# Kernel optimization log

Hardware: AMD Instinct MI355X
Metric: run time of the kernel (lower is better)

The kernel has to match this reference:

```python
import math
import jax, jax.numpy as jnp
import numpy as np

FIRE_THRESH = 0.85
DEPLETION_RATE = 0.5
EPS = 1e-12


def setup_inputs() -> dict:
    key = jax.random.key(0)
    k1, k2, k3, k4 = jax.random.split(key, 4)
    B, T, D, N = 8, 4096, 1024, 512
    x = jax.random.normal(k1, (B, T, D), dtype=jnp.float32)
    buf = jax.random.normal(k2, (N, D), dtype=jnp.float32)
    buf = buf / jnp.maximum(jnp.linalg.norm(buf, axis=-1, keepdims=True), EPS)
    depl = jax.random.uniform(k3, (N,), dtype=jnp.float32)
    hits = jax.random.randint(k4, (N,), 0, 5, dtype=jnp.int32)
    mask = jnp.ones((N,), dtype=bool)
    return {
        "x": x,
        "log_k": jnp.asarray(math.log(1.5), dtype=jnp.float32),
        "log_lambda": jnp.asarray(math.log(0.5), dtype=jnp.float32),
        "buf": buf,
        "depl": depl,
        "hits": hits,
        "mask": mask,
        "ptr": 7,
    }


def _gelu(x):
    c = math.sqrt(2.0 / math.pi)
    return 0.5 * x * (1.0 + jnp.tanh(c * (x + 0.044715 * x * x * x)))


def reference(x, log_k, log_lambda, buf, depl, hits, mask, ptr):
    k_depl = jnp.clip(jnp.exp(log_k), 0.1, 5.0)
    lam = jnp.clip(jnp.exp(log_lambda), 0.1, 3.0)

    y = _gelu(x)  # [B,T,D]
    D = x.shape[-1]
    # detached mean activation over all tokens -> [D]
    m_curr = jax.lax.stop_gradient(y).reshape(-1, D).mean(0)

    m_n = m_curr / jnp.maximum(jnp.linalg.norm(m_curr), EPS)
    buf_n = buf / jnp.maximum(jnp.linalg.norm(buf, axis=-1, keepdims=True), EPS)
    sims = jnp.where(mask, buf_n @ m_n, -1.0)  # [N]
    nearest = jnp.argmax(sims)
    max_sim = sims[nearest]
    depl_level = depl[nearest]
    h = hits[nearest].astype(y.dtype)

    # .item()-based gate in torch => no gradient through gate
    gate = jax.lax.stop_gradient(
        jnp.exp(-k_depl * (1.0 - depl_level) - lam * h)
    )
    output = y * gate

    # state update (fire, then circular write at ptr)
    fired = max_sim > FIRE_THRESH
    new_depl = depl.at[nearest].multiply(jnp.where(fired, DEPLETION_RATE, 1.0))
    new_hits = hits.at[nearest].add(jnp.where(fired, 1, 0).astype(hits.dtype))
    new_buf = buf.at[ptr].set(m_n)
    new_depl = new_depl.at[ptr].set(1.0)
    new_hits = new_hits.at[ptr].set(0)
    new_mask = mask.at[ptr].set(True)
    return output, new_buf, new_depl, new_hits, new_mask
```

## Files before the change

kernel.cpp:

```cpp
#include <hip/hip_runtime.h>
#include <math.h>

#define BT 32768
#define DD 1024
#define NN 512
#define PP 1024

__device__ __forceinline__ float fast_gelu(float x) {
    float u = 0.7978845608028654f * (x + 0.044715f * x * x * x);
    float e = __expf(2.0f * u);
    float t = 1.0f - __fdividef(2.0f, e + 1.0f);
    return 0.5f * x * (1.0f + t);
}

__global__ __launch_bounds__(256) void k_partial(const float4* __restrict__ x4,
                                                 float4* __restrict__ part) {
    int t = threadIdx.x;
    float4 acc = make_float4(0.f, 0.f, 0.f, 0.f);
    for (int row = blockIdx.x; row < BT; row += PP) {
        float4 v = x4[row * (DD / 4) + t];
        acc.x += fast_gelu(v.x);
        acc.y += fast_gelu(v.y);
        acc.z += fast_gelu(v.z);
        acc.w += fast_gelu(v.w);
    }
    part[blockIdx.x * (DD / 4) + t] = acc;
}

__global__ __launch_bounds__(256) void k_reduce1(const float* __restrict__ part,
                                                 float* __restrict__ part2) {
    int g = blockIdx.x * 256 + threadIdx.x;
    int col = g & (DD - 1);
    int chunk = g >> 10;
    float s = 0.f;
    int r0 = chunk * (PP / 16);
    for (int r = r0; r < r0 + PP / 16; ++r) s += part[r * DD + col];
    part2[chunk * DD + col] = s;
}

__global__ __launch_bounds__(1024) void k_mean_norm(const float* __restrict__ part2,
                                                    float* __restrict__ m_mean,
                                                    float* __restrict__ m_n,
                                                    float* __restrict__ nm_out) {
    int c = threadIdx.x;
    float s = 0.f;
    for (int r = 0; r < 16; ++r) s += part2[r * DD + c];
    float m = s * (1.0f / 32768.0f);
    m_mean[c] = m;
    __shared__ float red[1024];
    red[c] = m * m;
    __syncthreads();
    for (int st = 512; st > 0; st >>= 1) {
        if (c < st) red[c] += red[c + st];
        __syncthreads();
    }
    float nm = sqrtf(red[0]);
    float denom = fmaxf(nm, 1e-12f);
    m_n[c] = m / denom;
    if (c == 0) nm_out[0] = nm;
}

__global__ __launch_bounds__(256) void k_sims(const float4* __restrict__ buf4,
                                              const float4* __restrict__ m4,
                                              float* __restrict__ dot,
                                              float* __restrict__ sq) {
    int n = blockIdx.x;
    int t = threadIdx.x;
    float4 b = buf4[n * (DD / 4) + t];
    float4 m = m4[t];
    float d = b.x * m.x + b.y * m.y + b.z * m.z + b.w * m.w;
    float q = b.x * b.x + b.y * b.y + b.z * b.z + b.w * b.w;
    __shared__ float rd[256], rq[256];
    rd[t] = d;
    rq[t] = q;
    __syncthreads();
    for (int st = 128; st > 0; st >>= 1) {
        if (t < st) { rd[t] += rd[t + st]; rq[t] += rq[t + st]; }
        __syncthreads();
    }
    if (t == 0) { dot[n] = rd[0]; sq[n] = rq[0]; }
}

__global__ __launch_bounds__(512) void k_state(const float* __restrict__ dot,
                                               const float* __restrict__ sq,
                                               const float* __restrict__ nm_p,
                                               const float* __restrict__ depl,
                                               const int* __restrict__ hits,
                                               const int* __restrict__ mask,
                                               const float* __restrict__ logk_p,
                                               const float* __restrict__ loglam_p,
                                               const int* __restrict__ ptr_p,
                                               float* __restrict__ out_depl,
                                               float* __restrict__ out_hits,
                                               float* __restrict__ out_mask,
                                               float* __restrict__ gate_p) {
    int n = threadIdx.x;
    float nm = fmaxf(nm_p[0], 1e-12f);
    float nb = fmaxf(sqrtf(sq[n]), 1e-12f);
    bool mk = mask[n] != 0;
    float sim = mk ? dot[n] / (nb * nm) : -1.0f;

    __shared__ float ssim[512];
    __shared__ int sidx[512];
    ssim[n] = sim;
    sidx[n] = n;
    __syncthreads();
    for (int st = 256; st > 0; st >>= 1) {
        if (n < st) {
            float s2 = ssim[n + st];
            int i2 = sidx[n + st];
            if (s2 > ssim[n] || (s2 == ssim[n] && i2 < sidx[n])) {
                ssim[n] = s2;
                sidx[n] = i2;
            }
        }
        __syncthreads();
    }

    __shared__ int s_near, s_fired;
    if (n == 0) {
        int nearest = sidx[0];
        float msim = ssim[0];
        float k_depl = fminf(fmaxf(expf(logk_p[0]), 0.1f), 5.0f);
        float lam = fminf(fmaxf(expf(loglam_p[0]), 0.1f), 3.0f);
        float g = expf(-k_depl * (1.0f - depl[nearest]) - lam * (float)hits[nearest]);
        s_near = nearest;
        s_fired = (msim > 0.85f) ? 1 : 0;
        gate_p[0] = g;
    }
    __syncthreads();

    int ptr = ptr_p[0];
    float nd = depl[n];
    int nh = hits[n];
    float nmsk = mk ? 1.0f : 0.0f;
    if (n == s_near && s_fired) { nd *= 0.5f; nh += 1; }
    if (n == ptr) { nd = 1.0f; nh = 0; nmsk = 1.0f; }
    out_depl[n] = nd;
    out_hits[n] = (float)nh;
    out_mask[n] = nmsk;
}

__global__ __launch_bounds__(256) void k_out(const float4* __restrict__ x4,
                                             float4* __restrict__ o4,
                                             const float* __restrict__ gate_p,
                                             int n4) {
    float g = gate_p[0];
    int stride = gridDim.x * blockDim.x;
    for (int i = blockIdx.x * blockDim.x + threadIdx.x; i < n4; i += stride) {
        float4 v = x4[i];
        float4 r;
        r.x = fast_gelu(v.x) * g;
        r.y = fast_gelu(v.y) * g;
        r.z = fast_gelu(v.z) * g;
        r.w = fast_gelu(v.w) * g;
        o4[i] = r;
    }
}

__global__ __launch_bounds__(256) void k_buf(const float4* __restrict__ buf4,
                                             const float4* __restrict__ mn4,
                                             const int* __restrict__ ptr_p,
                                             float4* __restrict__ out4) {
    int i = blockIdx.x * 256 + threadIdx.x;
    int row = i >> 8;
    float4 v = (row == ptr_p[0]) ? mn4[i & 255] : buf4[i];
    out4[i] = v;
}

extern "C" void kernel_launch(void* const* d_in, const int* in_sizes, int n_in,
                              void* d_out, int out_size, void* d_ws, size_t ws_size,
                              hipStream_t stream) {
    const float* x = (const float*)d_in[0];
    const float* log_k = (const float*)d_in[1];
    const float* log_lambda = (const float*)d_in[2];
    const float* buf = (const float*)d_in[3];
    const float* depl = (const float*)d_in[4];
    const int* hits = (const int*)d_in[5];
    const int* mask = (const int*)d_in[6];
    const int* ptr = (const int*)d_in[7];

    float* out = (float*)d_out;
    float* out_buf = out + 33554432;
    float* out_depl = out_buf + NN * DD;
    float* out_hits = out_depl + NN;
    float* out_mask = out_hits + NN;

    float* ws = (float*)d_ws;
    float* part2 = ws;
    float* m_mean = ws + 16384;
    float* m_n = ws + 17408;
    float* nm = ws + 18432;
    float* gate = ws + 18433;
    float* dot = ws + 18440;
    float* sq = ws + 18952;

    float* part = out;

    k_partial<<<dim3(PP), dim3(256), 0, stream>>>((const float4*)x, (float4*)part);
    k_reduce1<<<dim3(64), dim3(256), 0, stream>>>(part, part2);
    k_mean_norm<<<dim3(1), dim3(1024), 0, stream>>>(part2, m_mean, m_n, nm);
    k_sims<<<dim3(NN), dim3(256), 0, stream>>>((const float4*)buf, (const float4*)m_mean, dot, sq);
    k_state<<<dim3(1), dim3(512), 0, stream>>>(dot, sq, nm, depl, hits, mask,
                                               log_k, log_lambda, ptr,
                                               out_depl, out_hits, out_mask, gate);
    k_out<<<dim3(2048), dim3(256), 0, stream>>>((const float4*)x, (float4*)out, gate, 8388608);
    k_buf<<<dim3(512), dim3(256), 0, stream>>>((const float4*)buf, (const float4*)m_n, ptr,
                                               (float4*)out_buf);
}
```

Measured before the change: 103.7 us.

## Fuse reduction and state kernels with last-block atomics; merge output and buffer writes

Result: slower. 138.9 us (+33.9%).

```diff
diff --git a/kernel.cpp b/kernel.cpp
--- a/kernel.cpp
+++ b/kernel.cpp
@@ -5,6 +5,8 @@
 #define DD 1024
 #define NN 512
 #define PP 1024
+
+typedef float v4f __attribute__((ext_vector_type(4)));
 
 __device__ __forceinline__ float fast_gelu(float x) {
     float u = 0.7978845608028654f * (x + 0.044715f * x * x * x);
@@ -13,12 +15,20 @@
     return 0.5f * x * (1.0f + t);
 }
 
-__global__ __launch_bounds__(256) void k_partial(const float4* __restrict__ x4,
-                                                 float4* __restrict__ part) {
+__device__ __forceinline__ void nt_store4(v4f* p, v4f v) {
+    __builtin_nontemporal_store(v, p);
+}
+
+__global__ __launch_bounds__(256) void k_partial(const v4f* __restrict__ x4,
+                                                 v4f* __restrict__ part,
+                                                 int* __restrict__ cnts) {
+    if (blockIdx.x == 0 && threadIdx.x == 0) { cnts[0] = 0; cnts[1] = 0; }
     int t = threadIdx.x;
-    float4 acc = make_float4(0.f, 0.f, 0.f, 0.f);
-    for (int row = blockIdx.x; row < BT; row += PP) {
-        float4 v = x4[row * (DD / 4) + t];
+    v4f acc = {0.f, 0.f, 0.f, 0.f};
+    int base = blockIdx.x * 32 * (DD / 4) + t;
+    #pragma unroll 4
+    for (int k = 0; k < 32; ++k) {
+        v4f v = x4[base + k * (DD / 4)];
         acc.x += fast_gelu(v.x);
         acc.y += fast_gelu(v.y);
         acc.z += fast_gelu(v.z);
@@ -27,47 +37,84 @@
     part[blockIdx.x * (DD / 4) + t] = acc;
 }
 
-__global__ __launch_bounds__(256) void k_reduce1(const float* __restrict__ part,
-                                                 float* __restrict__ part2) {
-    int g = blockIdx.x * 256 + threadIdx.x;
-    int col = g & (DD - 1);
-    int chunk = g >> 10;
-    float s = 0.f;
-    int r0 = chunk * (PP / 16);
-    for (int r = r0; r < r0 + PP / 16; ++r) s += part[r * DD + col];
-    part2[chunk * DD + col] = s;
-}
-
-__global__ __launch_bounds__(1024) void k_mean_norm(const float* __restrict__ part2,
-                                                    float* __restrict__ m_mean,
-                                                    float* __restrict__ m_n,
-                                                    float* __restrict__ nm_out) {
-    int c = threadIdx.x;
-    float s = 0.f;
-    for (int r = 0; r < 16; ++r) s += part2[r * DD + c];
-    float m = s * (1.0f / 32768.0f);
-    m_mean[c] = m;
-    __shared__ float red[1024];
-    red[c] = m * m;
-    __syncthreads();
-    for (int st = 512; st > 0; st >>= 1) {
-        if (c < st) red[c] += red[c + st];
+__global__ __launch_bounds__(256) void k_reduce_mean(const float* __restrict__ part,
+                                                     float* __restrict__ part2,
+                                                     float* __restrict__ m_mean,
+                                                     float* __restrict__ m_n,
+                                                     float* __restrict__ nm_out,
+                                                     int* __restrict__ cnts) {
+    int t = threadIdx.x, j = blockIdx.x;
+    float a0 = 0, a1 = 0, a2 = 0, a3 = 0;
+    for (int r = 0; r < 16; ++r) {
+        const float* row = part + (j * 16 + r) * DD;
+        a0 += row[t];
+        a1 += row[t + 256];
+        a2 += row[t + 512];
+        a3 += row[t + 768];
+    }
+    part2[j * DD + t] = a0;
+    part2[j * DD + t + 256] = a1;
+    part2[j * DD + t + 512] = a2;
+    part2[j * DD + t + 768] = a3;
+    __threadfence();
+    __shared__ int sLast;
+    if (t == 0) {
+        int old = __hip_atomic_fetch_add(&cnts[0], 1, __ATOMIC_ACQ_REL, __HIP_MEMORY_SCOPE_AGENT);
+        sLast = (old == 63) ? 1 : 0;
+    }
+    __syncthreads();
+    if (!sLast) return;
+    __threadfence();
+    float s0 = 0, s1 = 0, s2 = 0, s3 = 0;
+    for (int jj = 0; jj < 64; ++jj) {
+        const float* row = part2 + jj * DD;
+        s0 += row[t];
+        s1 += row[t + 256];
+        s2 += row[t + 512];
+        s3 += row[t + 768];
+    }
+    const float inv = 1.0f / 32768.0f;
+    float m0 = s0 * inv, m1 = s1 * inv, m2 = s2 * inv, m3 = s3 * inv;
+    m_mean[t] = m0;
+    m_mean[t + 256] = m1;
+    m_mean[t + 512] = m2;
+    m_mean[t + 768] = m3;
+    __shared__ float red[256];
+    red[t] = m0 * m0 + m1 * m1 + m2 * m2 + m3 * m3;
+    __syncthreads();
+    for (int st = 128; st > 0; st >>= 1) {
+        if (t < st) red[t] += red[t + st];
         __syncthreads();
     }
     float nm = sqrtf(red[0]);
-    float denom = fmaxf(nm, 1e-12f);
-    m_n[c] = m / denom;
-    if (c == 0) nm_out[0] = nm;
-}
-
-__global__ __launch_bounds__(256) void k_sims(const float4* __restrict__ buf4,
-                                              const float4* __restrict__ m4,
-                                              float* __restrict__ dot,
-                                              float* __restrict__ sq) {
-    int n = blockIdx.x;
-    int t = threadIdx.x;
-    float4 b = buf4[n * (DD / 4) + t];
-    float4 m = m4[t];
+    float den = fmaxf(nm, 1e-12f);
+    m_n[t] = m0 / den;
+    m_n[t + 256] = m1 / den;
+    m_n[t + 512] = m2 / den;
+    m_n[t + 768] = m3 / den;
+    if (t == 0) nm_out[0] = nm;
+}
+
+__global__ __launch_bounds__(256) void k_sims_state(const v4f* __restrict__ buf4,
+                                                    const float* __restrict__ m_meanf,
+                                                    const float* __restrict__ nm_p,
+                                                    const float* __restrict__ depl,
+                                                    const int* __restrict__ hits,
+                                                    const int* __restrict__ mask,
+                                                    const float* __restrict__ logk,
+                                                    const float* __restrict__ loglam,
+                                                    const int* __restrict__ ptrp,
+                                                    float* __restrict__ dot,
+                                                    float* __restrict__ sq,
+                                                    float* __restrict__ out_depl,
+                                                    float* __restrict__ out_hits,
+                                                    float* __restrict__ out_mask,
+                                                    float* __restrict__ gate_p,
+                                                    int* __restrict__ cnts) {
+    int t = threadIdx.x, n = blockIdx.x;
+    const v4f* m4 = (const v4f*)m_meanf;
+    v4f b = buf4[n * (DD / 4) + t];
+    v4f m = m4[t];
     float d = b.x * m.x + b.y * m.y + b.z * m.z + b.w * m.w;
     float q = b.x * b.x + b.y * b.y + b.z * b.z + b.w * b.w;
     __shared__ float rd[256], rq[256];
@@ -79,93 +126,92 @@
         __syncthreads();
     }
     if (t == 0) { dot[n] = rd[0]; sq[n] = rq[0]; }
-}
-
-__global__ __launch_bounds__(512) void k_state(const float* __restrict__ dot,
-                                               const float* __restrict__ sq,
-                                               const float* __restrict__ nm_p,
-                                               const float* __restrict__ depl,
-                                               const int* __restrict__ hits,
-                                               const int* __restrict__ mask,
-                                               const float* __restrict__ logk_p,
-                                               const float* __restrict__ loglam_p,
-                                               const int* __restrict__ ptr_p,
-                                               float* __restrict__ out_depl,
-                                               float* __restrict__ out_hits,
-                                               float* __restrict__ out_mask,
-                                               float* __restrict__ gate_p) {
-    int n = threadIdx.x;
+    __threadfence();
+    __shared__ int sLast;
+    if (t == 0) {
+        int old = __hip_atomic_fetch_add(&cnts[1], 1, __ATOMIC_ACQ_REL, __HIP_MEMORY_SCOPE_AGENT);
+        sLast = (old == NN - 1) ? 1 : 0;
+    }
+    __syncthreads();
+    if (!sLast) return;
+    __threadfence();
+
     float nm = fmaxf(nm_p[0], 1e-12f);
-    float nb = fmaxf(sqrtf(sq[n]), 1e-12f);
-    bool mk = mask[n] != 0;
-    float sim = mk ? dot[n] / (nb * nm) : -1.0f;
-
-    __shared__ float ssim[512];
-    __shared__ int sidx[512];
-    ssim[n] = sim;
-    sidx[n] = n;
-    __syncthreads();
-    for (int st = 256; st > 0; st >>= 1) {
-        if (n < st) {
-            float s2 = ssim[n + st];
-            int i2 = sidx[n + st];
-            if (s2 > ssim[n] || (s2 == ssim[n] && i2 < sidx[n])) {
-                ssim[n] = s2;
-                sidx[n] = i2;
-            }
+    float sA = mask[t] ? dot[t] / (fmaxf(sqrtf(sq[t]), 1e-12f) * nm) : -1.0f;
+    float sB = mask[t + 256] ? dot[t + 256] / (fmaxf(sqrtf(sq[t + 256]), 1e-12f) * nm) : -1.0f;
+    float bs;
+    int bi;
+    if (sB > sA) { bs = sB; bi = t + 256; } else { bs = sA; bi = t; }
+    __shared__ float sv[256];
+    __shared__ int si[256];
+    sv[t] = bs;
+    si[t] = bi;
+    __syncthreads();
+    for (int st = 128; st > 0; st >>= 1) {
+        if (t < st) {
+            float o = sv[t + st];
+            int oi = si[t + st];
+            if (o > sv[t] || (o == sv[t] && oi < si[t])) { sv[t] = o; si[t] = oi; }
         }
         __syncthreads();
     }
-
     __shared__ int s_near, s_fired;
-    if (n == 0) {
-        int nearest = sidx[0];
-        float msim = ssim[0];
-        float k_depl = fminf(fmaxf(expf(logk_p[0]), 0.1f), 5.0f);
-        float lam = fminf(fmaxf(expf(loglam_p[0]), 0.1f), 3.0f);
-        float g = expf(-k_depl * (1.0f - depl[nearest]) - lam * (float)hits[nearest]);
+    if (t == 0) {
+        int nearest = si[0];
+        float msim = sv[0];
+        float k_depl = fminf(fmaxf(expf(logk[0]), 0.1f), 5.0f);
+        float lam = fminf(fmaxf(expf(loglam[0]), 0.1f), 3.0f);
+        gate_p[0] = expf(-k_depl * (1.0f - depl[nearest]) - lam * (float)hits[nearest]);
         s_near = nearest;
         s_fired = (msim > 0.85f) ? 1 : 0;
-        gate_p[0] = g;
-    }
-    __syncthreads();
-
-    int ptr = ptr_p[0];
-    float nd = depl[n];
-    int nh = hits[n];
-    float nmsk = mk ? 1.0f : 0.0f;
-    if (n == s_near && s_fired) { nd *= 0.5f; nh += 1; }
-    if (n == ptr) { nd = 1.0f; nh = 0; nmsk = 1.0f; }
-    out_depl[n] = nd;
-    out_hits[n] = (float)nh;
-    out_mask[n] = nmsk;
-}
-
-__global__ __launch_bounds__(256) void k_out(const float4* __restrict__ x4,
-                                             float4* __restrict__ o4,
-                                             const float* __restrict__ gate_p,
-                                             int n4) {
-    float g = gate_p[0];
-    int stride = gridDim.x * blockDim.x;
-    for (int i = blockIdx.x * blockDim.x + threadIdx.x; i < n4; i += stride) {
-        float4 v = x4[i];
-        float4 r;
-        r.x = fast_gelu(v.x) * g;
-        r.y = fast_gelu(v.y) * g;
-        r.z = fast_gelu(v.z) * g;
-        r.w = fast_gelu(v.w) * g;
-        o4[i] = r;
-    }
-}
-
-__global__ __launch_bounds__(256) void k_buf(const float4* __restrict__ buf4,
-                                             const float4* __restrict__ mn4,
-                                             const int* __restrict__ ptr_p,
-                                             float4* __restrict__ out4) {
-    int i = blockIdx.x * 256 + threadIdx.x;
-    int row = i >> 8;
-    float4 v = (row == ptr_p[0]) ? mn4[i & 255] : buf4[i];
-    out4[i] = v;
+    }
+    __syncthreads();
+    int ptr = ptrp[0];
+    for (int k = 0; k < 2; ++k) {
+        int nn = t + k * 256;
+        float ndv = depl[nn];
+        int nh = hits[nn];
+        float nmsk = mask[nn] ? 1.0f : 0.0f;
+        if (nn == s_near && s_fired) { ndv *= 0.5f; nh += 1; }
+        if (nn == ptr) { ndv = 1.0f; nh = 0; nmsk = 1.0f; }
+        out_depl[nn] = ndv;
+        out_hits[nn] = (float)nh;
+        out_mask[nn] = nmsk;
+    }
+}
+
+__global__ __launch_bounds__(256) void k_outbuf(const v4f* __restrict__ x4,
+                                                v4f* __restrict__ o4,
+                                                const v4f* __restrict__ buf4,
+                                                const v4f* __restrict__ mn4,
+                                                v4f* __restrict__ ob4,
+                                                const float* __restrict__ gate_p,
+                                                const int* __restrict__ ptrp) {
+    int t = threadIdx.x;
+    if (blockIdx.x < 2048) {
+        float g = gate_p[0];
+        int base = blockIdx.x * 4096 + t;
+        #pragma unroll 4
+        for (int k = 0; k < 16; ++k) {
+            int i = base + k * 256;
+            v4f v = x4[i];
+            v4f r;
+            r.x = fast_gelu(v.x) * g;
+            r.y = fast_gelu(v.y) * g;
+            r.z = fast_gelu(v.z) * g;
+            r.w = fast_gelu(v.w) * g;
+            nt_store4(&o4[i], r);
+        }
+    } else {
+        int b2 = blockIdx.x - 2048;
+        int ptr = ptrp[0];
+        for (int k = 0; k < 16; ++k) {
+            int i = b2 * 4096 + k * 256 + t;
+            int row = i >> 8;
+            v4f v = (row == ptr) ? mn4[i & 255] : buf4[i];
+            ob4[i] = v;
+        }
+    }
 }
 
 extern "C" void kernel_launch(void* const* d_in, const int* in_sizes, int n_in,
@@ -186,25 +232,25 @@
     float* out_hits = out_depl + NN;
     float* out_mask = out_hits + NN;
 
-    float* ws = (float*)d_ws;
-    float* part2 = ws;
-    float* m_mean = ws + 16384;
-    float* m_n = ws + 17408;
-    float* nm = ws + 18432;
-    float* gate = ws + 18433;
-    float* dot = ws + 18440;
-    float* sq = ws + 18952;
+    int* cnts = (int*)d_ws;
+    float* wsf = (float*)d_ws;
+    float* m_mean = wsf + 16;
+    float* m_n = wsf + 1040;
+    float* nm = wsf + 2064;
+    float* gate = wsf + 2065;
+    float* dot = wsf + 2080;
+    float* sq = wsf + 2592;
 
     float* part = out;
-
-    k_partial<<<dim3(PP), dim3(256), 0, stream>>>((const float4*)x, (float4*)part);
-    k_reduce1<<<dim3(64), dim3(256), 0, stream>>>(part, part2);
-    k_mean_norm<<<dim3(1), dim3(1024), 0, stream>>>(part2, m_mean, m_n, nm);
-    k_sims<<<dim3(NN), dim3(256), 0, stream>>>((const float4*)buf, (const float4*)m_mean, dot, sq);
-    k_state<<<dim3(1), dim3(512), 0, stream>>>(dot, sq, nm, depl, hits, mask,
-                                               log_k, log_lambda, ptr,
-                                               out_depl, out_hits, out_mask, gate);
-    k_out<<<dim3(2048), dim3(256), 0, stream>>>((const float4*)x, (float4*)out, gate, 8388608);
-    k_buf<<<dim3(512), dim3(256), 0, stream>>>((const float4*)buf, (const float4*)m_n, ptr,
-                                               (float4*)out_buf);
-}
+    float* part2 = out + 16777216;
+
+    k_partial<<<dim3(PP), dim3(256), 0, stream>>>((const v4f*)x, (v4f*)part, cnts);
+    k_reduce_mean<<<dim3(64), dim3(256), 0, stream>>>(part, part2, m_mean, m_n, nm, cnts);
+    k_sims_state<<<dim3(NN), dim3(256), 0, stream>>>((const v4f*)buf, m_mean, nm, depl, hits,
+                                                     mask, log_k, log_lambda, ptr,
+                                                     dot, sq, out_depl, out_hits, out_mask,
+                                                     gate, cnts);
+    k_outbuf<<<dim3(2080), dim3(256), 0, stream>>>((const v4f*)x, (v4f*)out,
+                                                   (const v4f*)buf, (const v4f*)m_n,
+                                                   (v4f*)out_buf, gate, ptr);
+}
```
